# Kernel optimization log

Measured on AMD Instinct MI355X. Metric: run time of the kernel, lower is better.

## Reference

```python
import jax, jax.numpy as jnp
import numpy as np

N, F_IN, HID, C, H = 4096, 1024, 64, 40, 8
ALPHA = 0.2  # LeakyReLU negative slope
NEG_INF = -9e15

def setup_inputs() -> dict:
    key = jax.random.key(0)
    ks = jax.random.split(key, 8)
    x = jax.random.normal(ks[0], (N, F_IN), jnp.float32)
    adj = jax.random.randint(ks[1], (N, N), 0, 2, jnp.int32)  # dense 0/1 adjacency
    W = jax.random.normal(ks[2], (H, F_IN, HID), jnp.float32) / np.sqrt(F_IN).astype(np.float32)
    a_src = jax.random.normal(ks[3], (H, HID), jnp.float32) * 0.1
    a_dst = jax.random.normal(ks[4], (H, HID), jnp.float32) * 0.1
    W_out = jax.random.normal(ks[5], (H * HID, C), jnp.float32) / np.sqrt(H * HID).astype(np.float32)
    ao_src = jax.random.normal(ks[6], (C,), jnp.float32) * 0.1
    ao_dst = jax.random.normal(ks[7], (C,), jnp.float32) * 0.1
    return dict(x=x, adj=adj, W=W, a_src=a_src, a_dst=a_dst,
                W_out=W_out, ao_src=ao_src, ao_dst=ao_dst)

def _masked_attention(src, dst, mask):
    # src: [..., N] scores for row node i; dst: [..., N] scores for col node j
    e = jax.nn.leaky_relu(src[..., :, None] + dst[..., None, :], ALPHA)  # [..., N, N]
    e = jnp.where(mask, e, NEG_INF)
    return jax.nn.softmax(e, axis=-1)

def reference(x, adj, W, a_src, a_dst, W_out, ao_src, ao_dst):
    mask = adj > 0  # [N, N]
    # multi-head GAT layer (concat=True)
    Wh = jnp.einsum('nf,hfo->hno', x, W)            # [H, N, HID]
    src = jnp.einsum('hno,ho->hn', Wh, a_src)       # [H, N]
    dst = jnp.einsum('hno,ho->hn', Wh, a_dst)       # [H, N]
    att = _masked_attention(src, dst, mask[None])   # [H, N, N]
    h = jnp.einsum('hij,hjo->hio', att, Wh)         # [H, N, HID]
    h = jax.nn.elu(h)                               # concat=True -> elu inside layer
    h = jnp.transpose(h, (1, 0, 2)).reshape(N, H * HID)  # concat heads -> [N, H*HID]
    # output GAT layer (concat=False -> no elu inside)
    Wh2 = h @ W_out                                 # [N, C]
    att2 = _masked_attention(Wh2 @ ao_src, Wh2 @ ao_dst, mask)  # [N, N]
    out = att2 @ Wh2                                # [N, C]
    # model-level: elu then log_softmax over classes
    return jax.nn.log_softmax(jax.nn.elu(out), axis=1)
```

## Files before the change

kernel.cpp:

```cpp
#include <hip/hip_runtime.h>

#define NN 4096
#define F_IN 1024
#define NHEAD 8
#define HID 64
#define NCLS 40
#define LOG2E 1.44269504f

typedef float f32x4 __attribute__((ext_vector_type(4)));
typedef float f32x2 __attribute__((ext_vector_type(2)));
typedef short s16x8 __attribute__((ext_vector_type(8)));

#define SWZ(r,c) (((r)*64) + ((c) ^ (((r)&7)<<3)))

__device__ __forceinline__ unsigned short f2bf(float f){
  unsigned u = __float_as_uint(f);
  return (unsigned short)((u + 0x7fffu + ((u >> 16) & 1u)) >> 16);
}
__device__ __forceinline__ unsigned cvtpk(float lo, float hi){
  unsigned r; asm("v_cvt_pk_bf16_f32 %0, %1, %2" : "=v"(r) : "v"(lo), "v"(hi)); return r;
}
__device__ __forceinline__ f32x2 pkmul(f32x2 a, f32x2 b){
  f32x2 r; asm("v_pk_mul_f32 %0, %1, %2" : "=v"(r) : "v"(a), "v"(b)); return r;
}

__global__ __launch_bounds__(256) void pack_adj_k(const int* __restrict__ adj, unsigned* __restrict__ bmT){
  int gid = blockIdx.x*256 + threadIdx.x;
  int lane = threadIdx.x & 63;
  unsigned long long m = __ballot(adj[gid] > 0);
  int w = gid >> 5, i = w >> 7, jw = w & 127;
  if (lane == 0)       bmT[(size_t)jw*NN + i] = (unsigned)m;
  else if (lane == 32) bmT[(size_t)jw*NN + i] = (unsigned)(m >> 32);
}

__global__ __launch_bounds__(256) void cast_W_k(const float* __restrict__ W, unsigned short* __restrict__ WbT){
  __shared__ float T[64][65];
  const int h = blockIdx.y, k0 = blockIdx.x*64, t = threadIdx.x;
  for (int idx = t; idx < 1024; idx += 256){
    int k = idx >> 4, c4 = idx & 15;
    *(float4*)&T[k][c4*4] = *(const float4*)&W[((size_t)h*F_IN + k0 + k)*HID + c4*4];
  }
  __syncthreads();
  for (int idx = t; idx < 512; idx += 256){
    int o = idx >> 3, ch = idx & 7;
    s16x8 v;
    #pragma unroll
    for (int e = 0; e < 8; ++e) v[e] = (short)f2bf(T[ch*8 + e][o]);
    *(s16x8*)&WbT[((size_t)h*HID + o)*F_IN + k0 + ch*8] = v;
  }
}

__global__ __launch_bounds__(256) void cast_Wo_k(const float* __restrict__ Wout, unsigned short* __restrict__ WoT){
  int idx = blockIdx.x*256 + threadIdx.x;
  int cc = idx >> 9, k = idx & 511;
  WoT[idx] = (cc < NCLS) ? f2bf(Wout[(size_t)k*NCLS + cc]) : (unsigned short)0;
}

__global__ __launch_bounds__(256) void gemm1_k(const float* __restrict__ x,
    const unsigned short* __restrict__ WbT, unsigned short* __restrict__ WhT,
    const float* __restrict__ a_src, const float* __restrict__ a_dst,
    float* __restrict__ srcv, float* __restrict__ dstv){
  __shared__ unsigned short xS[64*64];
  __shared__ unsigned short wS[64*64];
  const int t = threadIdx.x, l = t & 63, wv = t >> 6, g = l >> 4, c = l & 15;
  const int h = blockIdx.y, n0 = blockIdx.x * 64;
  f32x4 acc[4] = {};
  for (int k0 = 0; k0 < F_IN; k0 += 64){
    __syncthreads();
    #pragma unroll
    for (int p = 0; p < 4; ++p){
      int idx = t + p*256, row = idx >> 4, c4 = idx & 15;
      float4 v = *(const float4*)&x[(size_t)(n0+row)*F_IN + k0 + c4*4];
      *(uint2*)&xS[SWZ(row, c4*4)] = make_uint2(cvtpk(v.x, v.y), cvtpk(v.z, v.w));
    }
    #pragma unroll
    for (int p = 0; p < 2; ++p){
      int idx = t + p*256, o = idx >> 3, ch = idx & 7;
      *(s16x8*)&wS[SWZ(o, ch*8)] = *(const s16x8*)&WbT[(size_t)(h*HID + o)*F_IN + k0 + ch*8];
    }
    __syncthreads();
    #pragma unroll
    for (int ks = 0; ks < 2; ++ks){
      s16x8 av = *(const s16x8*)&xS[SWZ(wv*16 + c, ks*32 + g*8)];
      #pragma unroll
      for (int ct = 0; ct < 4; ++ct){
        s16x8 bv = *(const s16x8*)&wS[SWZ(ct*16 + c, ks*32 + g*8)];
        acc[ct] = __builtin_amdgcn_mfma_f32_16x16x32_bf16(av, bv, acc[ct], 0, 0, 0);
      }
    }
  }
  float asv[4], adv[4];
  #pragma unroll
  for (int ct = 0; ct < 4; ++ct){ asv[ct] = a_src[h*HID + ct*16 + c]; adv[ct] = a_dst[h*HID + ct*16 + c]; }
  #pragma unroll
  for (int r = 0; r < 4; ++r){
    float ps = acc[0][r]*asv[0] + acc[1][r]*asv[1] + acc[2][r]*asv[2] + acc[3][r]*asv[3];
    float pd = acc[0][r]*adv[0] + acc[1][r]*adv[1] + acc[2][r]*adv[2] + acc[3][r]*adv[3];
    #pragma unroll
    for (int off = 1; off < 16; off <<= 1){ ps += __shfl_xor(ps, off); pd += __shfl_xor(pd, off); }
    if (c == 0){ int n = n0 + wv*16 + g*4 + r; srcv[h*NN + n] = ps; dstv[h*NN + n] = pd; }
  }
  __syncthreads();
  #pragma unroll
  for (int ct = 0; ct < 4; ++ct)
    *(uint2*)&xS[SWZ(ct*16 + c, wv*16 + g*4)] = make_uint2(cvtpk(acc[ct][0], acc[ct][1]), cvtpk(acc[ct][2], acc[ct][3]));
  __syncthreads();
  #pragma unroll
  for (int p = 0; p < 2; ++p){
    int idx = t + p*256, o = idx >> 3, ch = idx & 7;
    *(s16x8*)&WhT[(size_t)(h*HID + o)*NN + n0 + ch*8] = *(const s16x8*)&xS[SWZ(o, ch*8)];
  }
}

__global__ __launch_bounds__(256) void maxred_k(const float* __restrict__ in, float* __restrict__ out){
  __shared__ float red[4];
  const float* p = in + (size_t)blockIdx.x*NN;
  float m = -3.0e38f;
  for (int i = threadIdx.x; i < NN; i += 256) m = fmaxf(m, p[i]);
  #pragma unroll
  for (int off = 32; off; off >>= 1) m = fmaxf(m, __shfl_xor(m, off));
  if ((threadIdx.x & 63) == 0) red[threadIdx.x >> 6] = m;
  __syncthreads();
  if (threadIdx.x == 0) out[blockIdx.x] = fmaxf(fmaxf(red[0], red[1]), fmaxf(red[2], red[3]));
}

template<int NCT, int NJT, bool CHUNKED, bool DO_ELU>
__global__ __launch_bounds__(256) void agg_mfma_k(
    const unsigned* __restrict__ bmT, const unsigned short* __restrict__ VT,
    const float* __restrict__ srcv, const float* __restrict__ dstv,
    const float* __restrict__ maxp, void* __restrict__ outp)
{
  __shared__ unsigned short vS[2][NCT*16*64];
  __shared__ float2 dS[2][64];
  __shared__ unsigned bitS[2][2][32];
  const int t = threadIdx.x, l = t & 63, wv = t >> 6, g = l >> 4, c = l & 15;
  const int h   = CHUNKED ? 0 : blockIdx.y;
  const int jt0 = CHUNKED ? blockIdx.y * NJT : 0;
  const int i0 = blockIdx.x * 32;
  const int tl = wv >> 1, rH = wv & 1;
  const int lr = rH*16 + c;
  const float sr = srcv[h*NN + i0 + lr];
  const float mx = maxp[CHUNKED ? 0 : h];
  const float tm = sr + mx;
  const float mi2 = fmaxf(tm, 0.2f*tm) * LOG2E;
  f32x2 ac2;
  ac2[0] = exp2f(fmaf(sr, LOG2E, -mi2));
  ac2[1] = exp2f(fmaf(0.2f*sr, LOG2E, -mi2));
  const unsigned short* vb = VT + (size_t)h*HID*NN;

  f32x4 acc[NCT] = {};
  f32x4 accs = {};
  s16x8 ones;
  #pragma unroll
  for (int e = 0; e < 8; ++e) ones[e] = (short)0x3F80;

  s16x8 vreg[NCT]; float2 dreg = make_float2(0.f, 0.f); unsigned breg = 0;
  auto loadRegs = [&](int jt){
    #pragma unroll
    for (int p = 0; p < NCT; ++p){
      int u = t + p*256;
      int tt = u / (NCT*128), rem = u % (NCT*128);
      int o = rem >> 3, chk = rem & 7;
      vreg[p] = *(const s16x8*)&vb[(size_t)o*NN + (jt+tt)*64 + chk*8];
    }
    if (t < 128){
      float d = dstv[h*NN + (jt + (t>>6))*64 + (t&63)];
      dreg = make_float2(exp2f(d*LOG2E), exp2f(0.2f*d*LOG2E));
    }
    else { int u = t - 128; breg = bmT[(size_t)((jt + (u>>6))*2 + ((u>>5)&1))*NN + i0 + (u&31)]; }
  };
  auto writeLDS = [&](){
    #pragma unroll
    for (int p = 0; p < NCT; ++p){
      int u = t + p*256;
      int tt = u / (NCT*128), rem = u % (NCT*128);
      int o = rem >> 3, chk = rem & 7;
      *(s16x8*)&vS[tt][SWZ(o, chk*8)] = vreg[p];
    }
    if (t < 128) dS[t>>6][t&63] = dreg;
    else { int u = t - 128; bitS[u>>6][(u>>5)&1][u&31] = breg; }
  };

  loadRegs(jt0);
  for (int jj = 0; jj < NJT; jj += 2){
    __syncthreads();
    writeLDS();
    __syncthreads();
    if (jj + 2 < NJT) loadRegs(jt0 + jj + 2);
    #pragma unroll
    for (int ks = 0; ks < 2; ++ks){
      unsigned wb = (bitS[tl][ks][lr] >> (g*8)) & 0xffu;
      const f32x2* dr = (const f32x2*)&dS[tl][ks*32 + g*8];
      float q[8];
      #pragma unroll
      for (int e = 0; e < 8; ++e){
        f32x2 pr = pkmul(ac2, dr[e]);
        float m3 = __builtin_amdgcn_fmed3f(pr[0], pr[1], 1.0f);
        q[e] = (wb & (1u << e)) ? m3 : 0.f;
      }
      s16x8 af;
      ((unsigned*)&af)[0] = cvtpk(q[0], q[1]);
      ((unsigned*)&af)[1] = cvtpk(q[2], q[3]);
      ((unsigned*)&af)[2] = cvtpk(q[4], q[5]);
      ((unsigned*)&af)[3] = cvtpk(q[6], q[7]);
      #pragma unroll
      for (int ct = 0; ct < NCT; ++ct){
        s16x8 bv = *(const s16x8*)&vS[tl][SWZ(ct*16 + c, ks*32 + g*8)];
        acc[ct] = __builtin_amdgcn_mfma_f32_16x16x32_bf16(af, bv, acc[ct], 0, 0, 0);
      }
      accs = __builtin_amdgcn_mfma_f32_16x16x32_bf16(af, ones, accs, 0, 0, 0);
    }
  }
  __syncthreads();
  float* mrg = (float*)&vS[0][0];
  constexpr int S = (NCT + 1) * 4;
  if (tl == 1){
    int base = (rH*64 + l) * S;
    #pragma unroll
    for (int ct = 0; ct < NCT; ++ct)
      #pragma unroll
      for (int r = 0; r < 4; ++r) mrg[base + ct*4 + r] = acc[ct][r];
    #pragma unroll
    for (int r = 0; r < 4; ++r) mrg[base + NCT*4 + r] = accs[r];
  }
  __syncthreads();
  if (tl == 0){
    int base = (rH*64 + l) * S;
    #pragma unroll
    for (int ct = 0; ct < NCT; ++ct)
      #pragma unroll
      for (int r = 0; r < 4; ++r) acc[ct][r] += mrg[base + ct*4 + r];
    #pragma unroll
    for (int r = 0; r < 4; ++r) accs[r] += mrg[base + NCT*4 + r];
    if (!CHUNKED){
      unsigned short* ob = (unsigned short*)outp;
      #pragma unroll
      for (int r = 0; r < 4; ++r){
        float inv = 1.f / fmaxf(accs[r], 1e-30f);
        int row = i0 + rH*16 + g*4 + r;
        #pragma unroll
        for (int ct = 0; ct < NCT; ++ct){
          float v = acc[ct][r] * inv;
          if (DO_ELU) v = v > 0.f ? v : __expf(v) - 1.f;
          ob[(size_t)row*(NHEAD*HID) + h*HID + ct*16 + c] = f2bf(v);
        }
      }
    } else {
      float* ob = (float*)outp + (size_t)blockIdx.y * NN * 64;
      #pragma unroll
      for (int r = 0; r < 4; ++r){
        int row = i0 + rH*16 + g*4 + r;
        #pragma unroll
        for (int ct = 0; ct < NCT; ++ct)
          ob[(size_t)row*64 + ct*16 + c] = acc[ct][r];
        if (c == 0) ob[(size_t)row*64 + 48] = accs[r];
      }
    }
  }
}

__global__ __launch_bounds__(256) void gemm2_k(const unsigned short* __restrict__ hb,
    const unsigned short* __restrict__ WoT, const float* __restrict__ aos, const float* __restrict__ aod,
    unsigned short* __restrict__ WhT2, float* __restrict__ s2, float* __restrict__ d2){
  __shared__ unsigned short aS[64*64];
  __shared__ unsigned short bS[48*64];
  const int t = threadIdx.x, l = t & 63, wv = t >> 6, g = l >> 4, c = l & 15;
  const int n0 = blockIdx.x * 64;
  f32x4 acc[3] = {};
  for (int k0 = 0; k0 < NHEAD*HID; k0 += 64){
    __syncthreads();
    #pragma unroll
    for (int p = 0; p < 2; ++p){
      int u = t + p*256, o = u >> 3, ch = u & 7;
      *(s16x8*)&aS[SWZ(o, ch*8)] = *(const s16x8*)&hb[(size_t)(n0+o)*(NHEAD*HID) + k0 + ch*8];
    }
    for (int u = t; u < 384; u += 256){
      int o = u >> 3, ch = u & 7;
      *(s16x8*)&bS[SWZ(o, ch*8)] = *(const s16x8*)&WoT[(size_t)o*(NHEAD*HID) + k0 + ch*8];
    }
    __syncthreads();
    #pragma unroll
    for (int ks = 0; ks < 2; ++ks){
      s16x8 av = *(const s16x8*)&aS[SWZ(wv*16 + c, ks*32 + g*8)];
      #pragma unroll
      for (int ct = 0; ct < 3; ++ct){
        s16x8 bv = *(const s16x8*)&bS[SWZ(ct*16 + c, ks*32 + g*8)];
        acc[ct] = __builtin_amdgcn_mfma_f32_16x16x32_bf16(av, bv, acc[ct], 0, 0, 0);
      }
    }
  }
  float asv[3], adv[3];
  #pragma unroll
  for (int ct = 0; ct < 3; ++ct){
    int col = ct*16 + c;
    asv[ct] = (col < NCLS) ? aos[col] : 0.f;
    adv[ct] = (col < NCLS) ? aod[col] : 0.f;
  }
  #pragma unroll
  for (int r = 0; r < 4; ++r){
    float ps = acc[0][r]*asv[0] + acc[1][r]*asv[1] + acc[2][r]*asv[2];
    float pd = acc[0][r]*adv[0] + acc[1][r]*adv[1] + acc[2][r]*adv[2];
    #pragma unroll
    for (int off = 1; off < 16; off <<= 1){ ps += __shfl_xor(ps, off); pd += __shfl_xor(pd, off); }
    if (c == 0){ int n = n0 + wv*16 + g*4 + r; s2[n] = ps; d2[n] = pd; }
  }
  __syncthreads();
  #pragma unroll
  for (int ct = 0; ct < 3; ++ct)
    *(uint2*)&bS[SWZ(ct*16 + c, wv*16 + g*4)] = make_uint2(cvtpk(acc[ct][0], acc[ct][1]), cvtpk(acc[ct][2], acc[ct][3]));
  __syncthreads();
  for (int u = t; u < 384; u += 256){
    int o = u >> 3, ch = u & 7;
    *(s16x8*)&WhT2[(size_t)o*NN + n0 + ch*8] = *(const s16x8*)&bS[SWZ(o, ch*8)];
  }
}

__global__ __launch_bounds__(256) void final_k(const float* __restrict__ part, float* __restrict__ out){
  const int wid = (blockIdx.x*256 + threadIdx.x) >> 6;
  const int c = threadIdx.x & 63;
  float acc = 0.f, rs = 0.f;
  #pragma unroll
  for (int ch = 0; ch < 8; ++ch){
    const float* pb = part + ((size_t)ch*NN + wid)*64;
    if (c < 48) acc += pb[c];
    rs += pb[48];
  }
  float v = acc / fmaxf(rs, 1e-30f);
  float e = v > 0.f ? v : __expf(v) - 1.f;
  float ev = (c < NCLS) ? e : -3.0e38f;
  float m = ev;
  #pragma unroll
  for (int off = 32; off; off >>= 1) m = fmaxf(m, __shfl_xor(m, off));
  float ex = (c < NCLS) ? __expf(e - m) : 0.f;
  float s = ex;
  #pragma unroll
  for (int off = 32; off; off >>= 1) s += __shfl_xor(s, off);
  if (c < NCLS) out[(size_t)wid*NCLS + c] = e - m - __logf(s);
}

extern "C" void kernel_launch(void* const* d_in, const int* in_sizes, int n_in,
                              void* d_out, int out_size, void* d_ws, size_t ws_size,
                              hipStream_t stream){
  (void)in_sizes; (void)n_in; (void)out_size; (void)ws_size;
  const float* x     = (const float*)d_in[0];
  const int*   adj   = (const int*)  d_in[1];
  const float* W     = (const float*)d_in[2];
  const float* a_src = (const float*)d_in[3];
  const float* a_dst = (const float*)d_in[4];
  const float* W_out = (const float*)d_in[5];
  const float* aos   = (const float*)d_in[6];
  const float* aod   = (const float*)d_in[7];
  float* out = (float*)d_out;

  char* p = (char*)d_ws;
  unsigned* bmT        = (unsigned*)p;       p += (size_t)NN*128*4;
  unsigned short* WbT  = (unsigned short*)p; p += (size_t)NHEAD*HID*F_IN*2;
  unsigned short* WhT  = (unsigned short*)p; p += (size_t)NHEAD*HID*NN*2;
  unsigned short* hbuf = (unsigned short*)p; p += (size_t)NN*NHEAD*HID*2;
  unsigned short* WoT  = (unsigned short*)p; p += (size_t)48*NHEAD*HID*2;
  unsigned short* WhT2 = (unsigned short*)p; p += (size_t)48*NN*2;
  float* srcv = (float*)p; p += (size_t)NHEAD*NN*4;
  float* dstv = (float*)p; p += (size_t)NHEAD*NN*4;
  float* maxd = (float*)p; p += 256;
  float* s2   = (float*)p; p += (size_t)NN*4;
  float* d2   = (float*)p; p += (size_t)NN*4;
  float* m2   = (float*)p; p += 256;
  float* part = (float*)p; p += (size_t)8*NN*64*4;

  pack_adj_k<<<(NN*NN)/256, 256, 0, stream>>>(adj, bmT);
  cast_W_k<<<dim3(F_IN/64, NHEAD), 256, 0, stream>>>(W, WbT);
  cast_Wo_k<<<96, 256, 0, stream>>>(W_out, WoT);
  gemm1_k<<<dim3(NN/64, NHEAD), 256, 0, stream>>>(x, WbT, WhT, a_src, a_dst, srcv, dstv);
  maxred_k<<<NHEAD, 256, 0, stream>>>(dstv, maxd);
  agg_mfma_k<4, 64, false, true><<<dim3(NN/32, NHEAD), 256, 0, stream>>>(bmT, WhT, srcv, dstv, maxd, hbuf);
  gemm2_k<<<NN/64, 256, 0, stream>>>(hbuf, WoT, aos, aod, WhT2, s2, d2);
  maxred_k<<<1, 256, 0, stream>>>(d2, m2);
  agg_mfma_k<3, 8, true, false><<<dim3(NN/32, 8), 256, 0, stream>>>(bmT, WhT2, s2, d2, m2, part);
  final_k<<<NN/4, 256, 0, stream>>>(part, out);
}
```

Measured before the change: 159.8 us.

## Restructure aggregation kernel: per-wave column tiles, 64-row blocks, direct global V loads

The attention-aggregation kernel now processes 64 destination rows per block. Each wave independently walks its own subset of column tiles and holds accumulators for all four 16-row groups, so each loaded V fragment is reused across four MFMA row groups. V fragments are read straight from global memory into registers instead of being staged through shared memory, which removes the per-tile block-wide barriers. Only the per-wave dst and adjacency bits still pass through small double-buffered shared memory. The cost is a larger register footprint and a three-way cross-wave reduction at the end, and launch grids are halved to match.

```diff
diff --git a/kernel.cpp b/kernel.cpp
--- a/kernel.cpp
+++ b/kernel.cpp
@@ -130,131 +130,137 @@
     const float* __restrict__ srcv, const float* __restrict__ dstv,
     const float* __restrict__ maxp, void* __restrict__ outp)
 {
-  __shared__ unsigned short vS[2][NCT*16*64];
-  __shared__ float2 dS[2][64];
-  __shared__ unsigned bitS[2][2][32];
+  __shared__ float2 dS[4][2][64];
+  __shared__ unsigned bitS[4][2][2][64];
+  __shared__ float mrg[2][3][16][NCT*16 + 4];
   const int t = threadIdx.x, l = t & 63, wv = t >> 6, g = l >> 4, c = l & 15;
   const int h   = CHUNKED ? 0 : blockIdx.y;
   const int jt0 = CHUNKED ? blockIdx.y * NJT : 0;
-  const int i0 = blockIdx.x * 32;
-  const int tl = wv >> 1, rH = wv & 1;
-  const int lr = rH*16 + c;
-  const float sr = srcv[h*NN + i0 + lr];
+  const int i0 = blockIdx.x * 64;
   const float mx = maxp[CHUNKED ? 0 : h];
-  const float tm = sr + mx;
-  const float mi2 = fmaxf(tm, 0.2f*tm) * LOG2E;
-  f32x2 ac2;
-  ac2[0] = exp2f(fmaf(sr, LOG2E, -mi2));
-  ac2[1] = exp2f(fmaf(0.2f*sr, LOG2E, -mi2));
-  const unsigned short* vb = VT + (size_t)h*HID*NN;
-
-  f32x4 acc[NCT] = {};
-  f32x4 accs = {};
+  f32x2 ac2[4];
+  #pragma unroll
+  for (int af = 0; af < 4; ++af){
+    float sr = srcv[h*NN + i0 + af*16 + c];
+    float tm = sr + mx;
+    float mi2 = fmaxf(tm, 0.2f*tm) * LOG2E;
+    ac2[af][0] = exp2f(fmaf(sr, LOG2E, -mi2));
+    ac2[af][1] = exp2f(fmaf(0.2f*sr, LOG2E, -mi2));
+  }
+  const unsigned short* vb = VT + (CHUNKED ? (size_t)0 : (size_t)h*HID*NN);
+  const float* dp = dstv + (size_t)h*NN;
+
+  f32x4 acc[4][NCT] = {};
+  f32x4 accs[4] = {};
   s16x8 ones;
   #pragma unroll
   for (int e = 0; e < 8; ++e) ones[e] = (short)0x3F80;
 
-  s16x8 vreg[NCT]; float2 dreg = make_float2(0.f, 0.f); unsigned breg = 0;
-  auto loadRegs = [&](int jt){
-    #pragma unroll
-    for (int p = 0; p < NCT; ++p){
-      int u = t + p*256;
-      int tt = u / (NCT*128), rem = u % (NCT*128);
-      int o = rem >> 3, chk = rem & 7;
-      vreg[p] = *(const s16x8*)&vb[(size_t)o*NN + (jt+tt)*64 + chk*8];
-    }
-    if (t < 128){
-      float d = dstv[h*NN + (jt + (t>>6))*64 + (t&63)];
-      dreg = make_float2(exp2f(d*LOG2E), exp2f(0.2f*d*LOG2E));
-    }
-    else { int u = t - 128; breg = bmT[(size_t)((jt + (u>>6))*2 + ((u>>5)&1))*NN + i0 + (u&31)]; }
-  };
-  auto writeLDS = [&](){
-    #pragma unroll
-    for (int p = 0; p < NCT; ++p){
-      int u = t + p*256;
-      int tt = u / (NCT*128), rem = u % (NCT*128);
-      int o = rem >> 3, chk = rem & 7;
-      *(s16x8*)&vS[tt][SWZ(o, chk*8)] = vreg[p];
-    }
-    if (t < 128) dS[t>>6][t&63] = dreg;
-    else { int u = t - 128; bitS[u>>6][(u>>5)&1][u&31] = breg; }
-  };
-
-  loadRegs(jt0);
-  for (int jj = 0; jj < NJT; jj += 2){
-    __syncthreads();
-    writeLDS();
-    __syncthreads();
-    if (jj + 2 < NJT) loadRegs(jt0 + jj + 2);
+  float dcur = dp[(jt0 + wv)*64 + l];
+  unsigned b0 = bmT[(size_t)((jt0 + wv)*2 + 0)*NN + i0 + l];
+  unsigned b1 = bmT[(size_t)((jt0 + wv)*2 + 1)*NN + i0 + l];
+  int pp = 0;
+  for (int jt = jt0 + wv; jt < jt0 + NJT; jt += 4){
+    dS[wv][pp][l] = make_float2(exp2f(dcur*LOG2E), exp2f(0.2f*dcur*LOG2E));
+    bitS[wv][pp][0][l] = b0;
+    bitS[wv][pp][1][l] = b1;
+    if (jt + 4 < jt0 + NJT){
+      dcur = dp[(jt+4)*64 + l];
+      b0 = bmT[(size_t)((jt+4)*2 + 0)*NN + i0 + l];
+      b1 = bmT[(size_t)((jt+4)*2 + 1)*NN + i0 + l];
+    }
+    s16x8 bv[2][NCT];
+    #pragma unroll
+    for (int ks = 0; ks < 2; ++ks)
+      #pragma unroll
+      for (int ct = 0; ct < NCT; ++ct)
+        bv[ks][ct] = *(const s16x8*)&vb[(size_t)(ct*16 + c)*NN + jt*64 + ks*32 + g*8];
+    asm volatile("s_waitcnt lgkmcnt(0)" ::: "memory");
     #pragma unroll
     for (int ks = 0; ks < 2; ++ks){
-      unsigned wb = (bitS[tl][ks][lr] >> (g*8)) & 0xffu;
-      const f32x2* dr = (const f32x2*)&dS[tl][ks*32 + g*8];
-      float q[8];
-      #pragma unroll
-      for (int e = 0; e < 8; ++e){
-        f32x2 pr = pkmul(ac2, dr[e]);
-        float m3 = __builtin_amdgcn_fmed3f(pr[0], pr[1], 1.0f);
-        q[e] = (wb & (1u << e)) ? m3 : 0.f;
-      }
-      s16x8 af;
-      ((unsigned*)&af)[0] = cvtpk(q[0], q[1]);
-      ((unsigned*)&af)[1] = cvtpk(q[2], q[3]);
-      ((unsigned*)&af)[2] = cvtpk(q[4], q[5]);
-      ((unsigned*)&af)[3] = cvtpk(q[6], q[7]);
-      #pragma unroll
-      for (int ct = 0; ct < NCT; ++ct){
-        s16x8 bv = *(const s16x8*)&vS[tl][SWZ(ct*16 + c, ks*32 + g*8)];
-        acc[ct] = __builtin_amdgcn_mfma_f32_16x16x32_bf16(af, bv, acc[ct], 0, 0, 0);
-      }
-      accs = __builtin_amdgcn_mfma_f32_16x16x32_bf16(af, ones, accs, 0, 0, 0);
-    }
-  }
-  __syncthreads();
-  float* mrg = (float*)&vS[0][0];
-  constexpr int S = (NCT + 1) * 4;
-  if (tl == 1){
-    int base = (rH*64 + l) * S;
-    #pragma unroll
-    for (int ct = 0; ct < NCT; ++ct)
-      #pragma unroll
-      for (int r = 0; r < 4; ++r) mrg[base + ct*4 + r] = acc[ct][r];
-    #pragma unroll
-    for (int r = 0; r < 4; ++r) mrg[base + NCT*4 + r] = accs[r];
-  }
-  __syncthreads();
-  if (tl == 0){
-    int base = (rH*64 + l) * S;
-    #pragma unroll
-    for (int ct = 0; ct < NCT; ++ct)
-      #pragma unroll
-      for (int r = 0; r < 4; ++r) acc[ct][r] += mrg[base + ct*4 + r];
-    #pragma unroll
-    for (int r = 0; r < 4; ++r) accs[r] += mrg[base + NCT*4 + r];
-    if (!CHUNKED){
-      unsigned short* ob = (unsigned short*)outp;
-      #pragma unroll
-      for (int r = 0; r < 4; ++r){
-        float inv = 1.f / fmaxf(accs[r], 1e-30f);
-        int row = i0 + rH*16 + g*4 + r;
+      f32x2 drv[8];
+      #pragma unroll
+      for (int e = 0; e < 8; ++e) drv[e] = *(const f32x2*)&dS[wv][pp][ks*32 + g*8 + e];
+      #pragma unroll
+      for (int af = 0; af < 4; ++af){
+        unsigned wb = (bitS[wv][pp][ks][af*16 + c] >> (g*8)) & 0xffu;
+        float q[8];
         #pragma unroll
-        for (int ct = 0; ct < NCT; ++ct){
-          float v = acc[ct][r] * inv;
-          if (DO_ELU) v = v > 0.f ? v : __expf(v) - 1.f;
-          ob[(size_t)row*(NHEAD*HID) + h*HID + ct*16 + c] = f2bf(v);
+        for (int e = 0; e < 8; ++e){
+          f32x2 pr = pkmul(ac2[af], drv[e]);
+          float m3 = __builtin_amdgcn_fmed3f(pr[0], pr[1], 1.0f);
+          q[e] = (wb & (1u << e)) ? m3 : 0.f;
         }
-      }
-    } else {
-      float* ob = (float*)outp + (size_t)blockIdx.y * NN * 64;
-      #pragma unroll
-      for (int r = 0; r < 4; ++r){
-        int row = i0 + rH*16 + g*4 + r;
+        s16x8 afr;
+        ((unsigned*)&afr)[0] = cvtpk(q[0], q[1]);
+        ((unsigned*)&afr)[1] = cvtpk(q[2], q[3]);
+        ((unsigned*)&afr)[2] = cvtpk(q[4], q[5]);
+        ((unsigned*)&afr)[3] = cvtpk(q[6], q[7]);
         #pragma unroll
         for (int ct = 0; ct < NCT; ++ct)
-          ob[(size_t)row*64 + ct*16 + c] = acc[ct][r];
-        if (c == 0) ob[(size_t)row*64 + 48] = accs[r];
-      }
+          acc[af][ct] = __builtin_amdgcn_mfma_f32_16x16x32_bf16(afr, bv[ks][ct], acc[af][ct], 0, 0, 0);
+        accs[af] = __builtin_amdgcn_mfma_f32_16x16x32_bf16(afr, ones, accs[af], 0, 0, 0);
+      }
+    }
+    pp ^= 1;
+  }
+
+  __syncthreads();
+  #pragma unroll
+  for (int q2 = 0; q2 < 2; ++q2){
+    #pragma unroll
+    for (int af2 = 0; af2 < 2; ++af2){
+      int af = 2*q2 + af2;
+      if (wv != af){
+        int s = wv - (wv > af ? 1 : 0);
+        #pragma unroll
+        for (int ct = 0; ct < NCT; ++ct)
+          #pragma unroll
+          for (int r = 0; r < 4; ++r)
+            mrg[af2][s][g*4+r][ct*16+c] = acc[af][ct][r];
+        if (c == 0){
+          #pragma unroll
+          for (int r = 0; r < 4; ++r) mrg[af2][s][g*4+r][NCT*16] = accs[af][r];
+        }
+      }
+    }
+    __syncthreads();
+    if ((wv >> 1) == q2){
+      int af = wv, af2 = wv & 1;
+      #pragma unroll
+      for (int ct = 0; ct < NCT; ++ct)
+        #pragma unroll
+        for (int r = 0; r < 4; ++r)
+          acc[af][ct][r] += mrg[af2][0][g*4+r][ct*16+c] + mrg[af2][1][g*4+r][ct*16+c] + mrg[af2][2][g*4+r][ct*16+c];
+      #pragma unroll
+      for (int r = 0; r < 4; ++r)
+        accs[af][r] += mrg[af2][0][g*4+r][NCT*16] + mrg[af2][1][g*4+r][NCT*16] + mrg[af2][2][g*4+r][NCT*16];
+    }
+    __syncthreads();
+  }
+
+  if (!CHUNKED){
+    unsigned short* ob = (unsigned short*)outp;
+    #pragma unroll
+    for (int r = 0; r < 4; ++r){
+      float inv = 1.f / fmaxf(accs[wv][r], 1e-30f);
+      int row = i0 + wv*16 + g*4 + r;
+      #pragma unroll
+      for (int ct = 0; ct < NCT; ++ct){
+        float v = acc[wv][ct][r] * inv;
+        if (DO_ELU) v = v > 0.f ? v : __expf(v) - 1.f;
+        ob[(size_t)row*(NHEAD*HID) + h*HID + ct*16 + c] = f2bf(v);
+      }
+    }
+  } else {
+    float* ob = (float*)outp + (size_t)blockIdx.y * NN * 64;
+    #pragma unroll
+    for (int r = 0; r < 4; ++r){
+      int row = i0 + wv*16 + g*4 + r;
+      #pragma unroll
+      for (int ct = 0; ct < NCT; ++ct)
+        ob[(size_t)row*64 + ct*16 + c] = acc[wv][ct][r];
+      if (c == 0) ob[(size_t)row*64 + 48] = accs[wv][r];
     }
   }
 }
@@ -372,9 +378,9 @@
   cast_Wo_k<<<96, 256, 0, stream>>>(W_out, WoT);
   gemm1_k<<<dim3(NN/64, NHEAD), 256, 0, stream>>>(x, WbT, WhT, a_src, a_dst, srcv, dstv);
   maxred_k<<<NHEAD, 256, 0, stream>>>(dstv, maxd);
-  agg_mfma_k<4, 64, false, true><<<dim3(NN/32, NHEAD), 256, 0, stream>>>(bmT, WhT, srcv, dstv, maxd, hbuf);
+  agg_mfma_k<4, 64, false, true><<<dim3(NN/64, NHEAD), 256, 0, stream>>>(bmT, WhT, srcv, dstv, maxd, hbuf);
   gemm2_k<<<NN/64, 256, 0, stream>>>(hbuf, WoT, aos, aod, WhT2, s2, d2);
   maxred_k<<<1, 256, 0, stream>>>(d2, m2);
-  agg_mfma_k<3, 8, true, false><<<dim3(NN/32, 8), 256, 0, stream>>>(bmT, WhT2, s2, d2, m2, part);
+  agg_mfma_k<3, 8, true, false><<<dim3(NN/64, 8), 256, 0, stream>>>(bmT, WhT2, s2, d2, m2, part);
   final_k<<<NN/4, 256, 0, stream>>>(part, out);
 }
```

Result: slower. 174.3 us (+9.1%).
